# Kernel tuning notes

Hardware: AMD Instinct MI355X
Metric: run time of the kernel (lower is better)

Reference implementation:

```python
import jax, jax.numpy as jnp
import numpy as np

BS, SL, INDIM, D, H = 2, 2048, 1024, 64, 16
DH = D * H


def _rotation_buffers(sl, units):
    # int rotation_values branch: values=arange(sl), min_lam=1, max_lam=1000
    half = units // 2
    min_lam, max_lam = 1.0, 1000.0
    theta = min_lam / (2.0 * np.pi) * (max_lam / min_lam) ** (2.0 * np.arange(half) / units)
    pos = np.arange(sl, dtype=np.float64)[:, None] / theta[None]  # [sl, half]
    # tile([...,2]).reshape == repeat each entry twice along last dim -> [sl, units]
    rcos = np.repeat(np.cos(pos), 2, axis=-1).astype(np.float32)
    rsin = np.repeat(np.sin(pos), 2, axis=-1).astype(np.float32)
    return jnp.asarray(rcos), jnp.asarray(rsin)


def setup_inputs() -> dict:
    key = jax.random.key(0)
    ks = jax.random.split(key, 8)
    s = 0.02
    x = jax.random.normal(ks[0], (BS, SL, INDIM), jnp.float32)
    mask = jnp.zeros((BS, SL), jnp.float32)  # subtracted from logits; zeros = no masking
    Wqkv = jax.random.normal(ks[1], (INDIM, 3 * DH), jnp.float32) * s
    bqkv = jnp.zeros((3 * DH,), jnp.float32)
    Wo = jax.random.normal(ks[2], (DH, INDIM), jnp.float32) * s
    bo = jnp.zeros((INDIM,), jnp.float32)
    Wg = jax.random.normal(ks[3], (INDIM, DH), jnp.float32) * s
    bg = jnp.zeros((DH,), jnp.float32)
    Wb = jax.random.normal(ks[4], (INDIM, H), jnp.float32) * s
    bb = jnp.zeros((H,), jnp.float32)
    alphaq = jnp.zeros((), jnp.float32)
    alphak = jnp.zeros((), jnp.float32)
    alphav = jnp.zeros((), jnp.float32)
    rcos, rsin = _rotation_buffers(SL, D)
    return dict(x=x, mask=mask, Wqkv=Wqkv, bqkv=bqkv, Wo=Wo, bo=bo, Wg=Wg, bg=bg,
                Wb=Wb, bb=bb, alphaq=alphaq, alphak=alphak, alphav=alphav,
                rcos=rcos, rsin=rsin)


def _rotate(X, cos, sin_even):
    # Faithful to the in-place torch code:
    #   X_ = X*cos; X_[...,::2] += -sin[...,::2]*X_[...,1::2];
    #   X_[...,1::2] += sin[...,::2]*X_[...,::2]   (uses UPDATED even lanes)
    Xc = X * cos
    even = Xc[..., 0::2] - sin_even * Xc[..., 1::2]
    odd = Xc[..., 1::2] + sin_even * even
    return jnp.stack([even, odd], axis=-1).reshape(X.shape)


def reference(x, mask, Wqkv, bqkv, Wo, bo, Wg, bg, Wb, bb, alphaq, alphak, alphav, rcos, rsin):
    bs, sl, _ = x.shape
    qkv = x @ Wqkv + bqkv  # [bs, sl, 3*DH]
    Q, K, V = jnp.split(qkv, 3, axis=-1)
    # split last dim as (d, h) and move heads out: [bs, h, sl, d]
    def split_heads(t):
        return t.reshape(bs, sl, D, H).transpose(0, 3, 1, 2)
    Q = split_heads(Q) * jax.nn.sigmoid(alphaq)
    K = split_heads(K) * jax.nn.sigmoid(alphak)
    V = split_heads(V) * jax.nn.sigmoid(alphav)
    cos = rcos[:sl]            # [sl, d]
    sin_even = rsin[:sl, 0::2]  # [sl, d/2]
    Q = _rotate(Q, cos, sin_even)
    K = _rotate(K, cos, sin_even)
    scale = D ** (-0.5)
    QK = scale * jnp.einsum('bhqd,bhkd->bhqk', Q, K)  # [bs,h,sl,sl]
    # 'regular' bias: Wb(x) -> [bs,sl,h] -> [bs,h,1,sl] broadcast over queries
    B = (x @ Wb + bb)
    QK = QK + jnp.transpose(B, (0, 2, 1))[:, :, None, :]
    QK = QK - mask[:, None, None, :]
    w = jax.nn.softmax(QK, axis=-1)
    att = jnp.einsum('bhqk,bhkd->bhqd', w, V)  # [bs,h,sl,d]
    # sigmoid gate, split the same (d,h) way
    G = jax.nn.sigmoid(x @ Wg + bg).reshape(bs, sl, D, H).transpose(0, 3, 1, 2)
    att = att * G
    # merge heads back as (d, h) -> [bs, sl, d*h]
    att = att.transpose(0, 2, 3, 1).reshape(bs, sl, DH)
    resid = att @ Wo + bo
    return x + resid  # identity shortcut (out_units == indim), dropout=0
```

## Files before the change

### kernel.cpp

```cpp
#include <hip/hip_runtime.h>
#include <cstdint>

typedef unsigned short u16;
typedef unsigned int   u32;
typedef __bf16 bf16x8 __attribute__((ext_vector_type(8)));
typedef u16    u16x8  __attribute__((ext_vector_type(8)));
typedef float  f32x4  __attribute__((ext_vector_type(4)));
typedef float  f32x16 __attribute__((ext_vector_type(16)));
typedef u32    u32x2v __attribute__((ext_vector_type(2)));
typedef __attribute__((address_space(3))) void lds_void;
typedef __attribute__((address_space(1))) void gl_void;

#define GLDS16(gsrc, ldst) \
  __builtin_amdgcn_global_load_lds((gl_void*)(gsrc), (lds_void*)(ldst), 16, 0, 0)

#define DEV __device__ __forceinline__
#define LOG2E 1.4426950408889634f

DEV u16 f2bf(float f) {
  uint32_t u = __float_as_uint(f);
  u += 0x7fff + ((u >> 16) & 1);
  return (u16)(u >> 16);
}
DEV float bf2f(u16 h) { return __uint_as_float(((uint32_t)h) << 16); }
DEV float sigm(float x) { return 1.0f / (1.0f + __expf(-x)); }

__global__ __launch_bounds__(256) void cvtx_k(const float* __restrict__ x, u16* __restrict__ xb) {
  int i = blockIdx.x * 256 + threadIdx.x;
  float4 v = ((const float4*)x)[i];
  ushort4 o;
  o.x = f2bf(v.x); o.y = f2bf(v.y); o.z = f2bf(v.z); o.w = f2bf(v.w);
  ((ushort4*)xb)[i] = o;
}

template <int PERM>
__global__ __launch_bounds__(256) void wtransp_k(const float* __restrict__ W, u16* __restrict__ Wt,
                                                 int K, int N) {
  __shared__ float tile[32][33];
  int kt = blockIdx.x, nt = blockIdx.y;
  int t = threadIdx.x;
  int r = t >> 5, c = t & 31;
#pragma unroll
  for (int i = 0; i < 4; ++i)
    tile[r + i * 8][c] = W[(size_t)(kt * 32 + r + i * 8) * N + nt * 32 + c];
  __syncthreads();
#pragma unroll
  for (int i = 0; i < 4; ++i) {
    int ko = kt * 32 + c;
    int kdst = PERM ? ((ko & 15) * 64 + (ko >> 4)) : ko;
    Wt[(size_t)(nt * 32 + r + i * 8) * K + kdst] = f2bf(tile[c][r + i * 8]);
  }
}

__global__ __launch_bounds__(64) void biasb_k(const float* __restrict__ x, const float* __restrict__ Wb,
                                              const float* __restrict__ bb, const float* __restrict__ mask,
                                              float* __restrict__ bmT) {
  int row = blockIdx.x;
  int l = threadIdx.x;
  const float* xr = x + (size_t)row * 1024;
  float acc[16];
#pragma unroll
  for (int h = 0; h < 16; ++h) acc[h] = 0.f;
  for (int it = 0; it < 16; ++it) {
    int k = l + it * 64;
    float xv = xr[k];
    const float4* wr = (const float4*)(Wb + k * 16);
#pragma unroll
    for (int q = 0; q < 4; ++q) {
      float4 wv = wr[q];
      acc[q * 4 + 0] += xv * wv.x; acc[q * 4 + 1] += xv * wv.y;
      acc[q * 4 + 2] += xv * wv.z; acc[q * 4 + 3] += xv * wv.w;
    }
  }
#pragma unroll
  for (int h = 0; h < 16; ++h) {
    float v = acc[h];
#pragma unroll
    for (int m = 32; m >= 1; m >>= 1) v += __shfl_xor(v, m, 64);
    acc[h] = v;
  }
  if (l < 16) {
    int b = row >> 11, s = row & 2047;
    bmT[(size_t)(b * 16 + l) * 2048 + s] = (acc[l] + bb[l] - mask[row]) * LOG2E;
  }
}

__global__ __launch_bounds__(256) void gemmF_k(const u16* __restrict__ A, const u16* __restrict__ Bt,
                                               const float* __restrict__ bqkv, const float* __restrict__ bg,
                                               u16* __restrict__ qkvb, u16* __restrict__ gh_rm) {
  __shared__ u16 As[128 * 32];
  __shared__ u16 Bs[128 * 32];
  const int t = threadIdx.x, w = t >> 6, l = t & 63;
  const int lr = l & 15, lg = l >> 4;
  const int bm = blockIdx.x, bn = blockIdx.y;
  const int wr = w >> 1, wc = w & 1;
  f32x4 acc[4][4] = {};
  for (int kt = 0; kt < 32; ++kt) {
    if (kt) __syncthreads();
#pragma unroll
    for (int r = 0; r < 2; ++r) {
      int L = r * 256 + t;
      GLDS16(A + (size_t)(bm * 128 + (L >> 2)) * 1024 + (kt * 32 + (L & 3) * 8),
             &As[(r * 256 + w * 64) * 8]);
      GLDS16(Bt + (size_t)(bn * 128 + (L >> 2)) * 1024 + (kt * 32 + (L & 3) * 8),
             &Bs[(r * 256 + w * 64) * 8]);
    }
    __syncthreads();
    bf16x8 af[4], bfr[4];
#pragma unroll
    for (int m = 0; m < 4; ++m) af[m] = *(const bf16x8*)&As[(wr * 64 + m * 16 + lr) * 32 + lg * 8];
#pragma unroll
    for (int n = 0; n < 4; ++n) bfr[n] = *(const bf16x8*)&Bs[(wc * 64 + n * 16 + lr) * 32 + lg * 8];
#pragma unroll
    for (int m = 0; m < 4; ++m)
#pragma unroll
      for (int n = 0; n < 4; ++n)
        acc[m][n] = __builtin_amdgcn_mfma_f32_16x16x32_bf16(af[m], bfr[n], acc[m][n], 0, 0, 0);
  }
#pragma unroll
  for (int m = 0; m < 4; ++m)
#pragma unroll
    for (int n = 0; n < 4; ++n) {
      int col = bn * 128 + wc * 64 + n * 16 + lr;
      float bv = (bn < 24) ? bqkv[col] : bg[col - 3072];
#pragma unroll
      for (int rg = 0; rg < 4; ++rg) {
        int row = bm * 128 + wr * 64 + m * 16 + lg * 4 + rg;
        float v = acc[m][n][rg] + bv;
        if (bn < 24) qkvb[(size_t)row * 3072 + col] = f2bf(v);
        else         gh_rm[(size_t)row * 1024 + (col - 3072)] = f2bf(sigm(v));
      }
    }
}

__global__ __launch_bounds__(256) void relayout_k(const u16* __restrict__ qkv,
    const u16* __restrict__ gh_rm,
    const float* __restrict__ rcos, const float* __restrict__ rsin,
    const float* __restrict__ aq, const float* __restrict__ ak, const float* __restrict__ av,
    u16* __restrict__ Qh, u16* __restrict__ Kh, u16* __restrict__ Vh, u16* __restrict__ Gh) {
  int row = blockIdx.x;
  int b = row >> 11, s = row & 2047;
  int t = threadIdx.x;
  float sq = sigm(*aq) * 0.125f * LOG2E, sk = sigm(*ak), sv = sigm(*av);
  const u16* qrow = qkv + (size_t)row * 3072;
  if (t < 128) {
    int which = t >> 6;
    int idx = t & 63;
    int hoct = idx & 1, dp = idx >> 1;
    const u16* src = qrow + which * 1024;
    float sc = which ? sk : sq;
    u16* dst = which ? Kh : Qh;
    float cc = rcos[s * 64 + 2 * dp];
    float sn = rsin[s * 64 + 2 * dp];
    u16x8 Av = *(const u16x8*)(src + dp * 32 + hoct * 8);
    u16x8 Bv = *(const u16x8*)(src + dp * 32 + 16 + hoct * 8);
#pragma unroll
    for (int j = 0; j < 8; ++j) {
      float xe = bf2f(Av[j]) * sc, xo = bf2f(Bv[j]) * sc;
      float e = cc * xe - sn * (cc * xo);
      float o2 = cc * xo + sn * e;
      u32 pk = (u32)f2bf(e) | ((u32)f2bf(o2) << 16);
      *(u32*)&dst[((size_t)(b * 16 + hoct * 8 + j) * 2048 + s) * 64 + 2 * dp] = pk;
    }
  }
  {
    const u16* src = qrow + 2048;
    int h = t >> 4, d0 = (t & 15) * 4;
    ushort4 o4;
    o4.x = f2bf(bf2f(src[(d0 + 0) * 16 + h]) * sv);
    o4.y = f2bf(bf2f(src[(d0 + 1) * 16 + h]) * sv);
    o4.z = f2bf(bf2f(src[(d0 + 2) * 16 + h]) * sv);
    o4.w = f2bf(bf2f(src[(d0 + 3) * 16 + h]) * sv);
    *(ushort4*)&Vh[((size_t)(b * 16 + h) * 2048 + s) * 64 + d0] = o4;
  }
  {
    const u16* src = gh_rm + (size_t)row * 1024;
    int h = t >> 4, d0 = (t & 15) * 4;
    ushort4 o4;
    o4.x = src[(d0 + 0) * 16 + h];
    o4.y = src[(d0 + 1) * 16 + h];
    o4.z = src[(d0 + 2) * 16 + h];
    o4.w = src[(d0 + 3) * 16 + h];
    *(ushort4*)&Gh[((size_t)(b * 16 + h) * 2048 + s) * 64 + d0] = o4;
  }
}

__global__ __launch_bounds__(256, 4) void attn3_k(const u16* __restrict__ Qh, const u16* __restrict__ Kh,
    const u16* __restrict__ Vh, const float* __restrict__ bmT, const u16* __restrict__ Gh,
    u16* __restrict__ attg2) {
  __shared__ u16 smem[16384];
  u16* KsA  = smem;
  u16* VTsA = smem + 4096;
  u16* KsB  = smem + 8192;
  u16* VTsB = smem + 12288;
  const int t = threadIdx.x, w = t >> 6, l = t & 63;
  const int q32 = l & 31, hi = l >> 5;
  const int bid = blockIdx.x;
  const int xcd = bid & 7, j = bid >> 3;
  const int bh = xcd * 4 + (j & 3);
  const int qt64 = j >> 2;
  const int q32t = w >> 1, kvh = w & 1;
  const int q0w = qt64 * 64 + q32t * 32;

  bf16x8 qf[4];
  {
    const u16* qbase = Qh + ((size_t)bh * 2048 + q0w + q32) * 64 + hi * 8;
#pragma unroll
    for (int ks = 0; ks < 4; ++ks) qf[ks] = *(const bf16x8*)(qbase + ks * 16);
  }
  f32x16 o0 = {}, o1 = {};
  float mi = -1e30f, li = 0.f;

  u16* Ks  = kvh ? KsB : KsA;
  u16* VTs = kvh ? VTsB : VTsA;

  for (int i = 0; i < 16; ++i) {
    if (i) __syncthreads();
#pragma unroll
    for (int tile = 0; tile < 2; ++tile) {
      int ktg = tile * 16 + i;
      u16* KsT  = tile ? KsB : KsA;
      u16* VTsT = tile ? VTsB : VTsA;
#pragma unroll
      for (int r = 0; r < 2; ++r) {
        int L = r * 256 + t;
        int krow = L >> 3, kc = L & 7;
        GLDS16(Kh + ((size_t)bh * 2048 + ktg * 64 + krow) * 64 + ((kc ^ (krow & 7)) * 8),
               &KsT[(r * 256 + w * 64) * 8]);
      }
      {
        int kp = t >> 3, dc = t & 7;
        const u16* vsrc = Vh + ((size_t)bh * 2048 + ktg * 64 + kp * 2) * 64 + dc * 8;
        u16x8 v0 = *(const u16x8*)vsrc;
        u16x8 v1 = *(const u16x8*)(vsrc + 64);
#pragma unroll
        for (int jj = 0; jj < 8; ++jj) {
          int d = dc * 8 + jj;
          int sw = (d & 7) ^ ((d >> 3) & 7);
          *(u32*)((char*)VTsT + d * 128 + ((kp * 4) ^ (sw << 4))) = (u32)v0[jj] | ((u32)v1[jj] << 16);
        }
      }
    }
    __syncthreads();
    int kt = kvh * 16 + i;
    float bv0 = bmT[(size_t)bh * 2048 + kt * 64 + q32];
    float bv1 = bmT[(size_t)bh * 2048 + kt * 64 + 32 + q32];
#pragma unroll
    for (int sub = 0; sub < 2; ++sub) {
      f32x16 s = {};
#pragma unroll
      for (int ks = 0; ks < 4; ++ks) {
        bf16x8 kf = *(const bf16x8*)((const char*)Ks + (sub * 32 + q32) * 128 +
                                     (((2 * ks + hi) ^ (q32 & 7)) << 4));
        s = __builtin_amdgcn_mfma_f32_32x32x16_bf16(kf, qf[ks], s, 0, 0, 0);
      }
      {
        float bvs = sub ? bv1 : bv0;
        u32 bvb;
        asm("v_cvt_pk_bf16_f32 %0, %1, %2" : "=v"(bvb) : "v"(bvs), "v"(0.f));
        union { u32 wd[4]; bf16x8 v; } Ab = {}, Bb = {};
        Ab.wd[0] = hi ? 0u : bvb;
        Bb.wd[0] = hi ? 0u : 0x3F80u;
        s = __builtin_amdgcn_mfma_f32_32x32x16_bf16(Ab.v, Bb.v, s, 0, 0, 0);
      }
      float ma = fmaxf(fmaxf(s[0], s[1]), fmaxf(s[2], s[3]));
      float mb = fmaxf(fmaxf(s[4], s[5]), fmaxf(s[6], s[7]));
      float mc = fmaxf(fmaxf(s[8], s[9]), fmaxf(s[10], s[11]));
      float md = fmaxf(fmaxf(s[12], s[13]), fmaxf(s[14], s[15]));
      float tm = fmaxf(fmaxf(ma, mb), fmaxf(mc, md));
      tm = fmaxf(tm, __shfl_xor(tm, 32, 64));
      if (!__all(tm <= mi + 8.f)) {
        float mn = fmaxf(mi, tm);
        float fac = exp2f(mi - mn);
        mi = mn; li *= fac;
#pragma unroll
        for (int r = 0; r < 16; ++r) { o0[r] *= fac; o1[r] *= fac; }
      }
      float p[16];
#pragma unroll
      for (int r = 0; r < 16; ++r) p[r] = exp2f(s[r] - mi);
      float s0 = (p[0] + p[1]) + (p[2] + p[3]);
      float s1 = (p[4] + p[5]) + (p[6] + p[7]);
      float s2 = (p[8] + p[9]) + (p[10] + p[11]);
      float s3 = (p[12] + p[13]) + (p[14] + p[15]);
      li += (s0 + s1) + (s2 + s3);
      u32 c[8];
#pragma unroll
      for (int i2 = 0; i2 < 8; ++i2)
        asm("v_cvt_pk_bf16_f32 %0, %1, %2" : "=v"(c[i2]) : "v"(p[2 * i2]), "v"(p[2 * i2 + 1]));
      asm volatile("v_permlane32_swap_b32 %0, %1" : "+v"(c[0]), "+v"(c[2]));
      asm volatile("v_permlane32_swap_b32 %0, %1" : "+v"(c[1]), "+v"(c[3]));
      asm volatile("v_permlane32_swap_b32 %0, %1" : "+v"(c[4]), "+v"(c[6]));
      asm volatile("v_permlane32_swap_b32 %0, %1" : "+v"(c[5]), "+v"(c[7]));
      union { u32 wd[4]; bf16x8 v; } pf0, pf1;
      pf0.wd[0] = c[0]; pf0.wd[1] = c[1]; pf0.wd[2] = c[2]; pf0.wd[3] = c[3];
      pf1.wd[0] = c[4]; pf1.wd[1] = c[5]; pf1.wd[2] = c[6]; pf1.wd[3] = c[7];
#pragma unroll
      for (int ks2 = 0; ks2 < 2; ++ks2) {
        int chunk = sub * 4 + ks2 * 2 + hi;
        const bf16x8* pv = ks2 ? &pf1.v : &pf0.v;
        {
          int d = q32;
          int sw = (d & 7) ^ ((d >> 3) & 7);
          bf16x8 vf = *(const bf16x8*)((const char*)VTs + d * 128 + ((chunk ^ sw) << 4));
          o0 = __builtin_amdgcn_mfma_f32_32x32x16_bf16(vf, *pv, o0, 0, 0, 0);
        }
        {
          int d = 32 + q32;
          int sw = (d & 7) ^ ((d >> 3) & 7);
          bf16x8 vf = *(const bf16x8*)((const char*)VTs + d * 128 + ((chunk ^ sw) << 4));
          o1 = __builtin_amdgcn_mfma_f32_32x32x16_bf16(vf, *pv, o1, 0, 0, 0);
        }
      }
    }
  }
  li += __shfl_xor(li, 32, 64);
  __syncthreads();
  float* Of = (float*)smem + q32t * 2048;
  float* ml = (float*)smem + 4096;
  if (kvh == 0) {
#pragma unroll
    for (int r = 0; r < 16; ++r) {
      int d = (r & 3) + 8 * (r >> 2) + 4 * hi;
      Of[d * 32 + q32] = o0[r];
      Of[(d + 32) * 32 + q32] = o1[r];
    }
    if (hi == 0) { ml[q32t * 64 + q32] = mi; ml[q32t * 64 + 32 + q32] = li; }
  }
  __syncthreads();
  if (kvh == 1) {
    float m0 = ml[q32t * 64 + q32], l0 = ml[q32t * 64 + 32 + q32];
    float M = fmaxf(m0, mi);
    float e0 = exp2f(m0 - M), e1 = exp2f(mi - M);
    float inv = 1.f / (l0 * e0 + li * e1);
#pragma unroll
    for (int r = 0; r < 16; ++r) {
      int d = (r & 3) + 8 * (r >> 2) + 4 * hi;
      o0[r] = (Of[d * 32 + q32] * e0 + o0[r] * e1) * inv;
      o1[r] = (Of[(d + 32) * 32 + q32] * e0 + o1[r] * e1) * inv;
    }
    char* ob = (char*)Of;
#pragma unroll
    for (int dt = 0; dt < 2; ++dt) {
#pragma unroll
      for (int rq = 0; rq < 4; ++rq) {
        int dbase = rq * 8 + hi * 4 + dt * 32;
        float e0v = dt ? o1[rq * 4 + 0] : o0[rq * 4 + 0];
        float e1v = dt ? o1[rq * 4 + 1] : o0[rq * 4 + 1];
        float e2v = dt ? o1[rq * 4 + 2] : o0[rq * 4 + 2];
        float e3v = dt ? o1[rq * 4 + 3] : o0[rq * 4 + 3];
        u32 lo = (u32)f2bf(e0v) | ((u32)f2bf(e1v) << 16);
        u32 h2 = (u32)f2bf(e2v) | ((u32)f2bf(e3v) << 16);
        u32x2v val = {lo, h2};
        *(u32x2v*)(ob + q32 * 128 + ((dbase * 2) ^ ((q32 & 7) << 4))) = val;
      }
    }
    const u16* gbase = Gh + ((size_t)bh * 2048 + q0w) * 64;
    u16* abase = attg2 + ((size_t)bh * 2048 + q0w) * 64;
#pragma unroll
    for (int cc = 0; cc < 4; ++cc) {
      int off16 = cc * 64 + l;
      int q = off16 >> 3;
      int inner = (off16 & 7) << 4;
      u16x8 ov = *(const u16x8*)(ob + q * 128 + (inner ^ ((q & 7) << 4)));
      u16x8 gv = *(const u16x8*)(gbase + off16 * 8);
      u16x8 outv;
#pragma unroll
      for (int jj = 0; jj < 8; ++jj) outv[jj] = f2bf(bf2f(ov[jj]) * bf2f(gv[jj]));
      *(u16x8*)(abase + off16 * 8) = outv;
    }
  }
}

__global__ __launch_bounds__(256) void gemm2_k(const u16* __restrict__ A, const u16* __restrict__ Bt,
                                               const float* __restrict__ bo, const float* __restrict__ x,
                                               float* __restrict__ out) {
  __shared__ u16 As[64 * 32];
  __shared__ u16 Bs[128 * 32];
  const int t = threadIdx.x, w = t >> 6, l = t & 63;
  const int lr = l & 15, lg = l >> 4;
  const int bm = blockIdx.x, bn = blockIdx.y;
  const int wr = w >> 1, wc = w & 1;
  f32x4 acc[2][4] = {};
  for (int kt = 0; kt < 32; ++kt) {
    if (kt) __syncthreads();
    {
      int arow = bm * 64 + (t >> 2), ak = kt * 32 + (t & 3) * 8;
      size_t aoff = ((size_t)((arow >> 11) * 16 + (ak >> 6)) * 2048 + (arow & 2047)) * 64 + (ak & 63);
      GLDS16(A + aoff, &As[w * 64 * 8]);
    }
#pragma unroll
    for (int r = 0; r < 2; ++r) {
      int L = r * 256 + t;
      GLDS16(Bt + (size_t)(bn * 128 + (L >> 2)) * 1024 + (kt * 32 + (L & 3) * 8),
             &Bs[(r * 256 + w * 64) * 8]);
    }
    __syncthreads();
    bf16x8 af[2], bfr[4];
#pragma unroll
    for (int m = 0; m < 2; ++m) af[m] = *(const bf16x8*)&As[(wr * 32 + m * 16 + lr) * 32 + lg * 8];
#pragma unroll
    for (int n = 0; n < 4; ++n) bfr[n] = *(const bf16x8*)&Bs[(wc * 64 + n * 16 + lr) * 32 + lg * 8];
#pragma unroll
    for (int m = 0; m < 2; ++m)
#pragma unroll
      for (int n = 0; n < 4; ++n)
        acc[m][n] = __builtin_amdgcn_mfma_f32_16x16x32_bf16(af[m], bfr[n], acc[m][n], 0, 0, 0);
  }
#pragma unroll
  for (int m = 0; m < 2; ++m)
#pragma unroll
    for (int n = 0; n < 4; ++n) {
      int col = bn * 128 + wc * 64 + n * 16 + lr;
      float bv = bo[col];
#pragma unroll
      for (int rg = 0; rg < 4; ++rg) {
        int row = bm * 64 + wr * 32 + m * 16 + lg * 4 + rg;
        out[(size_t)row * 1024 + col] = acc[m][n][rg] + bv + x[(size_t)row * 1024 + col];
      }
    }
}

extern "C" void kernel_launch(void* const* d_in, const int* in_sizes, int n_in,
                              void* d_out, int out_size, void* d_ws, size_t ws_size,
                              hipStream_t stream) {
  (void)in_sizes; (void)n_in; (void)out_size; (void)ws_size;
  const float* x    = (const float*)d_in[0];
  const float* mask = (const float*)d_in[1];
  const float* Wqkv = (const float*)d_in[2];
  const float* bqkv = (const float*)d_in[3];
  const float* Wo   = (const float*)d_in[4];
  const float* bo   = (const float*)d_in[5];
  const float* Wg   = (const float*)d_in[6];
  const float* bg   = (const float*)d_in[7];
  const float* Wb   = (const float*)d_in[8];
  const float* bb   = (const float*)d_in[9];
  const float* aq   = (const float*)d_in[10];
  const float* ak   = (const float*)d_in[11];
  const float* av   = (const float*)d_in[12];
  const float* rcos = (const float*)d_in[13];
  const float* rsin = (const float*)d_in[14];
  float* out = (float*)d_out;

  char* ws = (char*)d_ws;
  size_t o = 0;
  u16* x_bf   = (u16*)(ws + o); o += (size_t)4096 * 1024 * 2;
  u16* wcat   = (u16*)(ws + o); o += (size_t)4096 * 1024 * 2;
  u16* wo_t2  = (u16*)(ws + o); o += (size_t)1024 * 1024 * 2;
  u16* qkv_b  = (u16*)(ws + o); o += (size_t)4096 * 3072 * 2;
  u16* gh_rm  = (u16*)(ws + o); o += (size_t)4096 * 1024 * 2;
  u16* Gh     = (u16*)(ws + o); o += (size_t)32 * 2048 * 64 * 2;
  u16* Qh     = (u16*)(ws + o); o += (size_t)32 * 2048 * 64 * 2;
  u16* Kh     = (u16*)(ws + o); o += (size_t)32 * 2048 * 64 * 2;
  u16* Vh     = (u16*)(ws + o); o += (size_t)32 * 2048 * 64 * 2;
  float* bmT  = (float*)(ws + o); o += (size_t)32 * 2048 * 4;
  u16* attg2  = (u16*)(ws + o); o += (size_t)4096 * 1024 * 2;

  cvtx_k<<<4096, 256, 0, stream>>>(x, x_bf);
  wtransp_k<0><<<dim3(32, 96), 256, 0, stream>>>(Wqkv, wcat, 1024, 3072);
  wtransp_k<0><<<dim3(32, 32), 256, 0, stream>>>(Wg, wcat + (size_t)3072 * 1024, 1024, 1024);
  wtransp_k<1><<<dim3(32, 32), 256, 0, stream>>>(Wo, wo_t2, 1024, 1024);
  biasb_k<<<4096, 64, 0, stream>>>(x, Wb, bb, mask, bmT);
  gemmF_k<<<dim3(32, 32), 256, 0, stream>>>(x_bf, wcat, bqkv, bg, qkv_b, gh_rm);
  relayout_k<<<4096, 256, 0, stream>>>(qkv_b, gh_rm, rcos, rsin, aq, ak, av, Qh, Kh, Vh, Gh);
  attn3_k<<<1024, 256, 0, stream>>>(Qh, Kh, Vh, bmT, Gh, attg2);
  gemm2_k<<<dim3(64, 8), 256, 0, stream>>>(attg2, wo_t2, bo, x, out);
}
```

Measured before the change: 304.3 us.

## Double-buffer GEMM and attention K/V staging, pre-transpose V globally

Both GEMMs and the attention kernel now prefetch the next k-tile into a second LDS buffer while the current one is consumed, with a single barrier per iteration. A new kernel writes V transposed to global memory so attention can stage V^T with async global-to-LDS copies instead of a register-level transpose. Attention now gives each wave its own 32-query block over all 64-key tiles, which removes the split-KV merge through shared memory but halves the grid to 512 blocks. It also uses a native exp2 builtin and reuses the Vh buffer for the attention output, at the cost of an extra launch and a global V^T round trip.

```diff
diff --git a/kernel.cpp b/kernel.cpp
--- a/kernel.cpp
+++ b/kernel.cpp
@@ -17,6 +17,15 @@
 #define DEV __device__ __forceinline__
 #define LOG2E 1.4426950408889634f
 
+#if defined(__has_builtin)
+#if __has_builtin(__builtin_amdgcn_exp2f)
+#define EXP2(x) __builtin_amdgcn_exp2f(x)
+#endif
+#endif
+#ifndef EXP2
+#define EXP2(x) exp2f(x)
+#endif
+
 DEV u16 f2bf(float f) {
   uint32_t u = __float_as_uint(f);
   u += 0x7fff + ((u >> 16) & 1);
@@ -88,15 +97,16 @@
 __global__ __launch_bounds__(256) void gemmF_k(const u16* __restrict__ A, const u16* __restrict__ Bt,
                                                const float* __restrict__ bqkv, const float* __restrict__ bg,
                                                u16* __restrict__ qkvb, u16* __restrict__ gh_rm) {
-  __shared__ u16 As[128 * 32];
-  __shared__ u16 Bs[128 * 32];
+  __shared__ u16 sAB[4][4096];
   const int t = threadIdx.x, w = t >> 6, l = t & 63;
   const int lr = l & 15, lg = l >> 4;
   const int bm = blockIdx.x, bn = blockIdx.y;
   const int wr = w >> 1, wc = w & 1;
   f32x4 acc[4][4] = {};
-  for (int kt = 0; kt < 32; ++kt) {
-    if (kt) __syncthreads();
+
+  auto stage = [&](int buf, int kt) {
+    u16* As = sAB[buf * 2];
+    u16* Bs = sAB[buf * 2 + 1];
 #pragma unroll
     for (int r = 0; r < 2; ++r) {
       int L = r * 256 + t;
@@ -105,7 +115,15 @@
       GLDS16(Bt + (size_t)(bn * 128 + (L >> 2)) * 1024 + (kt * 32 + (L & 3) * 8),
              &Bs[(r * 256 + w * 64) * 8]);
     }
-    __syncthreads();
+  };
+
+  stage(0, 0);
+  __syncthreads();
+  for (int kt = 0; kt < 32; ++kt) {
+    int buf = kt & 1;
+    if (kt < 31) stage(buf ^ 1, kt + 1);
+    const u16* As = sAB[buf * 2];
+    const u16* Bs = sAB[buf * 2 + 1];
     bf16x8 af[4], bfr[4];
 #pragma unroll
     for (int m = 0; m < 4; ++m) af[m] = *(const bf16x8*)&As[(wr * 64 + m * 16 + lr) * 32 + lg * 8];
@@ -116,6 +134,7 @@
 #pragma unroll
       for (int n = 0; n < 4; ++n)
         acc[m][n] = __builtin_amdgcn_mfma_f32_16x16x32_bf16(af[m], bfr[n], acc[m][n], 0, 0, 0);
+    __syncthreads();
   }
 #pragma unroll
   for (int m = 0; m < 4; ++m)
@@ -185,22 +204,45 @@
   }
 }
 
-__global__ __launch_bounds__(256, 4) void attn3_k(const u16* __restrict__ Qh, const u16* __restrict__ Kh,
-    const u16* __restrict__ Vh, const float* __restrict__ bmT, const u16* __restrict__ Gh,
+__global__ __launch_bounds__(256) void vtrans_k(const u16* __restrict__ Vh, u16* __restrict__ VTg) {
+  __shared__ u16 vt[4096];
+  int bh = blockIdx.x, kt = blockIdx.y;
+  int t = threadIdx.x;
+  {
+    int kp = t >> 3, dc = t & 7;
+    const u16* vsrc = Vh + ((size_t)bh * 2048 + kt * 64 + kp * 2) * 64 + dc * 8;
+    u16x8 v0 = *(const u16x8*)vsrc;
+    u16x8 v1 = *(const u16x8*)(vsrc + 64);
+#pragma unroll
+    for (int j = 0; j < 8; ++j) {
+      int d = dc * 8 + j;
+      int sw = (d & 7) ^ ((d >> 3) & 7);
+      *(u32*)((char*)vt + d * 128 + ((kp * 4) ^ (sw << 4))) = (u32)v0[j] | ((u32)v1[j] << 16);
+    }
+  }
+  __syncthreads();
+  {
+    int d = t >> 2, ch = t & 3;
+    int sw = (d & 7) ^ ((d >> 3) & 7);
+    u16x8 a = *(const u16x8*)((const char*)vt + d * 128 + ((ch ^ sw) << 4));
+    u16x8 b = *(const u16x8*)((const char*)vt + d * 128 + (((ch + 4) ^ sw) << 4));
+    u16* dst = VTg + ((size_t)bh * 64 + d) * 2048 + kt * 64;
+    *(u16x8*)(dst + ch * 8) = a;
+    *(u16x8*)(dst + (ch + 4) * 8) = b;
+  }
+}
+
+__global__ __launch_bounds__(256) void attn4_k(const u16* __restrict__ Qh, const u16* __restrict__ Kh,
+    const u16* __restrict__ VTg, const float* __restrict__ bmT, const u16* __restrict__ Gh,
     u16* __restrict__ attg2) {
   __shared__ u16 smem[16384];
-  u16* KsA  = smem;
-  u16* VTsA = smem + 4096;
-  u16* KsB  = smem + 8192;
-  u16* VTsB = smem + 12288;
   const int t = threadIdx.x, w = t >> 6, l = t & 63;
   const int q32 = l & 31, hi = l >> 5;
   const int bid = blockIdx.x;
-  const int xcd = bid & 7, j = bid >> 3;
-  const int bh = xcd * 4 + (j & 3);
-  const int qt64 = j >> 2;
-  const int q32t = w >> 1, kvh = w & 1;
-  const int q0w = qt64 * 64 + q32t * 32;
+  const int xcd = bid & 7, within = bid >> 3;
+  const int bh = xcd * 4 + (within & 3);
+  const int qt = within >> 2;
+  const int q0w = qt * 128 + w * 32;
 
   bf16x8 qf[4];
   {
@@ -211,38 +253,33 @@
   f32x16 o0 = {}, o1 = {};
   float mi = -1e30f, li = 0.f;
 
-  u16* Ks  = kvh ? KsB : KsA;
-  u16* VTs = kvh ? VTsB : VTsA;
-
-  for (int i = 0; i < 16; ++i) {
-    if (i) __syncthreads();
-#pragma unroll
-    for (int tile = 0; tile < 2; ++tile) {
-      int ktg = tile * 16 + i;
-      u16* KsT  = tile ? KsB : KsA;
-      u16* VTsT = tile ? VTsB : VTsA;
-#pragma unroll
-      for (int r = 0; r < 2; ++r) {
-        int L = r * 256 + t;
-        int krow = L >> 3, kc = L & 7;
-        GLDS16(Kh + ((size_t)bh * 2048 + ktg * 64 + krow) * 64 + ((kc ^ (krow & 7)) * 8),
-               &KsT[(r * 256 + w * 64) * 8]);
-      }
-      {
-        int kp = t >> 3, dc = t & 7;
-        const u16* vsrc = Vh + ((size_t)bh * 2048 + ktg * 64 + kp * 2) * 64 + dc * 8;
-        u16x8 v0 = *(const u16x8*)vsrc;
-        u16x8 v1 = *(const u16x8*)(vsrc + 64);
-#pragma unroll
-        for (int jj = 0; jj < 8; ++jj) {
-          int d = dc * 8 + jj;
-          int sw = (d & 7) ^ ((d >> 3) & 7);
-          *(u32*)((char*)VTsT + d * 128 + ((kp * 4) ^ (sw << 4))) = (u32)v0[jj] | ((u32)v1[jj] << 16);
-        }
-      }
-    }
-    __syncthreads();
-    int kt = kvh * 16 + i;
+  auto stage = [&](int buf, int kt) {
+    u16* KsT = smem + buf * 8192;
+    u16* VTsT = KsT + 4096;
+#pragma unroll
+    for (int r = 0; r < 2; ++r) {
+      int L = r * 256 + t;
+      int row = L >> 3, kc = L & 7;
+      GLDS16(Kh + ((size_t)bh * 2048 + kt * 64 + row) * 64 + ((kc ^ (row & 7)) * 8),
+             &KsT[(r * 256 + w * 64) * 8]);
+    }
+#pragma unroll
+    for (int r = 0; r < 2; ++r) {
+      int L = r * 256 + t;
+      int d = L >> 3, kc = L & 7;
+      GLDS16(VTg + ((size_t)bh * 64 + d) * 2048 + kt * 64 + ((kc ^ (d & 7)) * 8),
+             &VTsT[(r * 256 + w * 64) * 8]);
+    }
+  };
+
+  stage(0, 0);
+  __syncthreads();
+
+  for (int kt = 0; kt < 32; ++kt) {
+    int buf = kt & 1;
+    if (kt < 31) stage(buf ^ 1, kt + 1);
+    const u16* Ks = smem + buf * 8192;
+    const u16* VTs = Ks + 4096;
     float bv0 = bmT[(size_t)bh * 2048 + kt * 64 + q32];
     float bv1 = bmT[(size_t)bh * 2048 + kt * 64 + 32 + q32];
 #pragma unroll
@@ -263,22 +300,25 @@
         Bb.wd[0] = hi ? 0u : 0x3F80u;
         s = __builtin_amdgcn_mfma_f32_32x32x16_bf16(Ab.v, Bb.v, s, 0, 0, 0);
       }
-      float ma = fmaxf(fmaxf(s[0], s[1]), fmaxf(s[2], s[3]));
-      float mb = fmaxf(fmaxf(s[4], s[5]), fmaxf(s[6], s[7]));
-      float mc = fmaxf(fmaxf(s[8], s[9]), fmaxf(s[10], s[11]));
-      float md = fmaxf(fmaxf(s[12], s[13]), fmaxf(s[14], s[15]));
-      float tm = fmaxf(fmaxf(ma, mb), fmaxf(mc, md));
+      float tm = fmaxf(fmaxf(s[0], s[1]), s[2]);
+      tm = fmaxf(fmaxf(tm, s[3]), s[4]);
+      tm = fmaxf(fmaxf(tm, s[5]), s[6]);
+      tm = fmaxf(fmaxf(tm, s[7]), s[8]);
+      tm = fmaxf(fmaxf(tm, s[9]), s[10]);
+      tm = fmaxf(fmaxf(tm, s[11]), s[12]);
+      tm = fmaxf(fmaxf(tm, s[13]), s[14]);
+      tm = fmaxf(tm, s[15]);
       tm = fmaxf(tm, __shfl_xor(tm, 32, 64));
       if (!__all(tm <= mi + 8.f)) {
         float mn = fmaxf(mi, tm);
-        float fac = exp2f(mi - mn);
+        float fac = EXP2(mi - mn);
         mi = mn; li *= fac;
 #pragma unroll
         for (int r = 0; r < 16; ++r) { o0[r] *= fac; o1[r] *= fac; }
       }
       float p[16];
 #pragma unroll
-      for (int r = 0; r < 16; ++r) p[r] = exp2f(s[r] - mi);
+      for (int r = 0; r < 16; ++r) p[r] = EXP2(s[r] - mi);
       float s0 = (p[0] + p[1]) + (p[2] + p[3]);
       float s1 = (p[4] + p[5]) + (p[6] + p[7]);
       float s2 = (p[8] + p[9]) + (p[10] + p[11]);
@@ -301,45 +341,24 @@
         const bf16x8* pv = ks2 ? &pf1.v : &pf0.v;
         {
           int d = q32;
-          int sw = (d & 7) ^ ((d >> 3) & 7);
-          bf16x8 vf = *(const bf16x8*)((const char*)VTs + d * 128 + ((chunk ^ sw) << 4));
+          bf16x8 vf = *(const bf16x8*)((const char*)VTs + d * 128 + ((chunk ^ (d & 7)) << 4));
           o0 = __builtin_amdgcn_mfma_f32_32x32x16_bf16(vf, *pv, o0, 0, 0, 0);
         }
         {
           int d = 32 + q32;
-          int sw = (d & 7) ^ ((d >> 3) & 7);
-          bf16x8 vf = *(const bf16x8*)((const char*)VTs + d * 128 + ((chunk ^ sw) << 4));
+          bf16x8 vf = *(const bf16x8*)((const char*)VTs + d * 128 + ((chunk ^ (d & 7)) << 4));
           o1 = __builtin_amdgcn_mfma_f32_32x32x16_bf16(vf, *pv, o1, 0, 0, 0);
         }
       }
     }
+    __syncthreads();
   }
   li += __shfl_xor(li, 32, 64);
-  __syncthreads();
-  float* Of = (float*)smem + q32t * 2048;
-  float* ml = (float*)smem + 4096;
-  if (kvh == 0) {
-#pragma unroll
-    for (int r = 0; r < 16; ++r) {
-      int d = (r & 3) + 8 * (r >> 2) + 4 * hi;
-      Of[d * 32 + q32] = o0[r];
-      Of[(d + 32) * 32 + q32] = o1[r];
-    }
-    if (hi == 0) { ml[q32t * 64 + q32] = mi; ml[q32t * 64 + 32 + q32] = li; }
-  }
-  __syncthreads();
-  if (kvh == 1) {
-    float m0 = ml[q32t * 64 + q32], l0 = ml[q32t * 64 + 32 + q32];
-    float M = fmaxf(m0, mi);
-    float e0 = exp2f(m0 - M), e1 = exp2f(mi - M);
-    float inv = 1.f / (l0 * e0 + li * e1);
-#pragma unroll
-    for (int r = 0; r < 16; ++r) {
-      int d = (r & 3) + 8 * (r >> 2) + 4 * hi;
-      o0[r] = (Of[d * 32 + q32] * e0 + o0[r] * e1) * inv;
-      o1[r] = (Of[(d + 32) * 32 + q32] * e0 + o1[r] * e1) * inv;
-    }
-    char* ob = (char*)Of;
+  float inv = 1.f / li;
+#pragma unroll
+  for (int r = 0; r < 16; ++r) { o0[r] *= inv; o1[r] *= inv; }
+  {
+    char* ob = (char*)smem + w * 4096;
 #pragma unroll
     for (int dt = 0; dt < 2; ++dt) {
 #pragma unroll
@@ -375,37 +394,44 @@
 __global__ __launch_bounds__(256) void gemm2_k(const u16* __restrict__ A, const u16* __restrict__ Bt,
                                                const float* __restrict__ bo, const float* __restrict__ x,
                                                float* __restrict__ out) {
-  __shared__ u16 As[64 * 32];
-  __shared__ u16 Bs[128 * 32];
+  __shared__ u16 sA[2][2048];
+  __shared__ u16 sB[2][4096];
   const int t = threadIdx.x, w = t >> 6, l = t & 63;
   const int lr = l & 15, lg = l >> 4;
   const int bm = blockIdx.x, bn = blockIdx.y;
   const int wr = w >> 1, wc = w & 1;
   f32x4 acc[2][4] = {};
-  for (int kt = 0; kt < 32; ++kt) {
-    if (kt) __syncthreads();
+
+  auto stage = [&](int buf, int kt) {
     {
       int arow = bm * 64 + (t >> 2), ak = kt * 32 + (t & 3) * 8;
       size_t aoff = ((size_t)((arow >> 11) * 16 + (ak >> 6)) * 2048 + (arow & 2047)) * 64 + (ak & 63);
-      GLDS16(A + aoff, &As[w * 64 * 8]);
+      GLDS16(A + aoff, &sA[buf][w * 64 * 8]);
     }
 #pragma unroll
     for (int r = 0; r < 2; ++r) {
       int L = r * 256 + t;
       GLDS16(Bt + (size_t)(bn * 128 + (L >> 2)) * 1024 + (kt * 32 + (L & 3) * 8),
-             &Bs[(r * 256 + w * 64) * 8]);
-    }
-    __syncthreads();
+             &sB[buf][(r * 256 + w * 64) * 8]);
+    }
+  };
+
+  stage(0, 0);
+  __syncthreads();
+  for (int kt = 0; kt < 32; ++kt) {
+    int buf = kt & 1;
+    if (kt < 31) stage(buf ^ 1, kt + 1);
     bf16x8 af[2], bfr[4];
 #pragma unroll
-    for (int m = 0; m < 2; ++m) af[m] = *(const bf16x8*)&As[(wr * 32 + m * 16 + lr) * 32 + lg * 8];
-#pragma unroll
-    for (int n = 0; n < 4; ++n) bfr[n] = *(const bf16x8*)&Bs[(wc * 64 + n * 16 + lr) * 32 + lg * 8];
+    for (int m = 0; m < 2; ++m) af[m] = *(const bf16x8*)&sA[buf][(wr * 32 + m * 16 + lr) * 32 + lg * 8];
+#pragma unroll
+    for (int n = 0; n < 4; ++n) bfr[n] = *(const bf16x8*)&sB[buf][(wc * 64 + n * 16 + lr) * 32 + lg * 8];
 #pragma unroll
     for (int m = 0; m < 2; ++m)
 #pragma unroll
       for (int n = 0; n < 4; ++n)
         acc[m][n] = __builtin_amdgcn_mfma_f32_16x16x32_bf16(af[m], bfr[n], acc[m][n], 0, 0, 0);
+    __syncthreads();
   }
 #pragma unroll
   for (int m = 0; m < 2; ++m)
@@ -453,8 +479,9 @@
   u16* Qh     = (u16*)(ws + o); o += (size_t)32 * 2048 * 64 * 2;
   u16* Kh     = (u16*)(ws + o); o += (size_t)32 * 2048 * 64 * 2;
   u16* Vh     = (u16*)(ws + o); o += (size_t)32 * 2048 * 64 * 2;
+  u16* VTg    = (u16*)(ws + o); o += (size_t)32 * 64 * 2048 * 2;
   float* bmT  = (float*)(ws + o); o += (size_t)32 * 2048 * 4;
-  u16* attg2  = (u16*)(ws + o); o += (size_t)4096 * 1024 * 2;
+  u16* attg2  = Vh;
 
   cvtx_k<<<4096, 256, 0, stream>>>(x, x_bf);
   wtransp_k<0><<<dim3(32, 96), 256, 0, stream>>>(Wqkv, wcat, 1024, 3072);
@@ -463,6 +490,7 @@
   biasb_k<<<4096, 64, 0, stream>>>(x, Wb, bb, mask, bmT);
   gemmF_k<<<dim3(32, 32), 256, 0, stream>>>(x_bf, wcat, bqkv, bg, qkv_b, gh_rm);
   relayout_k<<<4096, 256, 0, stream>>>(qkv_b, gh_rm, rcos, rsin, aq, ak, av, Qh, Kh, Vh, Gh);
-  attn3_k<<<1024, 256, 0, stream>>>(Qh, Kh, Vh, bmT, Gh, attg2);
+  vtrans_k<<<dim3(32, 32), 256, 0, stream>>>(Vh, VTg);
+  attn4_k<<<512, 256, 0, stream>>>(Qh, Kh, VTg, bmT, Gh, attg2);
   gemm2_k<<<dim3(64, 8), 256, 0, stream>>>(attg2, wo_t2, bo, x, out);
 }
```

Result: no change. 299.2 us (-1.7%).
